# Optimization experiments

Hardware: AMD Instinct MI355X
Metric: run time of the kernel (lower is better)

Reference implementation:

```python
import jax, jax.numpy as jnp
import numpy as np

B, C, D, H, CS = 2, 1024, 512, 8, 64  # batch, bindings, d_binding, heads, chunk_size


def setup_inputs() -> dict:
    key = jax.random.key(0)
    ks = jax.random.split(key, 12)
    d = D // H
    def lin(k, out_f, in_f):
        return jax.random.normal(k, (out_f, in_f), jnp.float32) * (1.0 / np.sqrt(in_f))
    return {
        "x": jax.random.normal(ks[0], (B, C, D), jnp.float32),
        "Wq": lin(ks[1], D, D), "bq": jnp.zeros((D,), jnp.float32),
        "Wk": lin(ks[2], D, D), "bk": jnp.zeros((D,), jnp.float32),
        "Wv": lin(ks[3], D, D), "bv": jnp.zeros((D,), jnp.float32),
        "w1": lin(ks[4], d, 3 * d), "b1": jnp.zeros((d,), jnp.float32),
        "w2": lin(ks[5], 1, d), "b2": jnp.zeros((1,), jnp.float32),
        "Wo": lin(ks[6], D, D), "bo": jnp.zeros((D,), jnp.float32),
    }


def reference(x, Wq, bq, Wk, bk, Wv, bv, w1, b1, w2, b2, Wo, bo):
    Bx, Cx, Dx = x.shape
    d = Dx // H
    def heads(W, b):
        y = jnp.einsum('bcD,eD->bce', x, W) + b
        return y.reshape(Bx, Cx, H, d).transpose(0, 2, 1, 3)  # (B,H,C,d)
    q = heads(Wq, bq)
    k = heads(Wk, bk)
    v = heads(Wv, bv)
    # split first MLP layer weight into q / k / q*k blocks
    w1_q, w1_k, w1_qk = w1[:, :d], w1[:, d:2 * d], w1[:, 2 * d:]
    qp = jnp.einsum('bhcd,ed->bhce', q, w1_q)  # (B,H,C,d)
    kp = jnp.einsum('bhcd,ed->bhce', k, w1_k)  # (B,H,C,d)
    nc = Cx // CS
    q_ch = q.reshape(Bx, H, nc, CS, d).transpose(2, 0, 1, 3, 4)   # (nc,B,H,CS,d)
    qp_ch = qp.reshape(Bx, H, nc, CS, d).transpose(2, 0, 1, 3, 4)
    inv_sqrt_d = jnp.float32(1.0 / np.sqrt(d))

    def step(carry, xs):
        qc, qpc = xs  # (B,H,CS,d) each
        # hidden: (B,H,CS,C,d)
        res = qpc[:, :, :, None, :] + kp[:, :, None, :, :] + b1
        inter = qc[:, :, :, None, :] * k[:, :, None, :, :]
        hid = res + jnp.einsum('bhijd,ed->bhije', inter, w1_qk)
        h = jax.nn.gelu(hid, approximate=False)
        scores = (jnp.einsum('bhije,e->bhij', h, w2[0]) + b2[0]) * inv_sqrt_d
        attn = jax.nn.softmax(scores, axis=-1)  # (B,H,CS,C)
        out = jnp.einsum('bhij,bhjd->bhid', attn, v)  # (B,H,CS,d)
        return carry, out

    _, outs = jax.lax.scan(jax.checkpoint(step), None, (q_ch, qp_ch))  # (nc,B,H,CS,d)
    out = outs.transpose(1, 2, 0, 3, 4).reshape(Bx, H, Cx, d)
    out = out.transpose(0, 2, 1, 3).reshape(Bx, Cx, Dx)
    return jnp.einsum('bcD,eD->bce', out, Wo) + bo
```

## Files before the change

kernel.cpp:

```cpp
#include <hip/hip_runtime.h>
#include <cstdint>

typedef unsigned short u16;
typedef unsigned int u32;
typedef __attribute__((ext_vector_type(8))) short short8;
typedef __attribute__((ext_vector_type(4))) float floatx4;
typedef __attribute__((ext_vector_type(2))) float floatx2;

__device__ __forceinline__ float b2f(u16 u) {
    union { unsigned int i; float f; } c; c.i = ((unsigned int)u) << 16; return c.f;
}
__device__ __forceinline__ u16 f2b(float f) {
    union { float f; unsigned int i; } c; c.f = f;
    unsigned int u = c.i;
    u = u + 0x7FFFu + ((u >> 16) & 1u);
    return (u16)(u >> 16);
}
__device__ __forceinline__ float u2f(u32 u) { union { u32 u; float f; } c; c.u = u; return c.f; }

__device__ __forceinline__ void kstage(const u16* gsrc, u16* ldst) {
    __builtin_amdgcn_global_load_lds(
        (const __attribute__((address_space(1))) u32*)gsrc,
        (__attribute__((address_space(3))) u32*)ldst, 16, 0, 0);
}

__global__ __launch_bounds__(256) void gemm_qkv(
    const float* __restrict__ x,
    const float* __restrict__ Wq, const float* __restrict__ Wk, const float* __restrict__ Wv,
    const float* __restrict__ bq, const float* __restrict__ bk, const float* __restrict__ bv,
    float* __restrict__ qout, u16* __restrict__ kout,
    u16* __restrict__ vthi, u16* __restrict__ vtlo)
{
    __shared__ u16 xs[64 * 72];
    __shared__ u16 wsl[64 * 72];
    int tid = threadIdx.x;
    int lane = tid & 63;
    int wv = tid >> 6;
    int lo = lane & 15, hi = lane >> 4;
    int which = blockIdx.y >> 3;
    int m0 = blockIdx.x * 64, n0 = (blockIdx.y & 7) * 64;
    const float* W    = which == 0 ? Wq : (which == 1 ? Wk : Wv);
    const float* bias = which == 0 ? bq : (which == 1 ? bk : bv);

    floatx4 acc[4];
#pragma unroll
    for (int mt = 0; mt < 4; ++mt) acc[mt] = (floatx4){0.f, 0.f, 0.f, 0.f};

    for (int k0 = 0; k0 < 512; k0 += 64) {
        __syncthreads();
#pragma unroll
        for (int i = 0; i < 2; ++i) {
            int v = tid + i * 256;
            int row = v >> 3, c8 = (v & 7) * 8;
            const float* ap = x + (m0 + row) * 512 + k0 + c8;
            const float* wp = W + (n0 + row) * 512 + k0 + c8;
            float4 a0 = *(const float4*)(ap);
            float4 a1 = *(const float4*)(ap + 4);
            float4 w0 = *(const float4*)(wp);
            float4 w1v = *(const float4*)(wp + 4);
            union { u16 u[8]; uint4 q; } ca, cw;
            ca.u[0] = f2b(a0.x); ca.u[1] = f2b(a0.y); ca.u[2] = f2b(a0.z); ca.u[3] = f2b(a0.w);
            ca.u[4] = f2b(a1.x); ca.u[5] = f2b(a1.y); ca.u[6] = f2b(a1.z); ca.u[7] = f2b(a1.w);
            cw.u[0] = f2b(w0.x); cw.u[1] = f2b(w0.y); cw.u[2] = f2b(w0.z); cw.u[3] = f2b(w0.w);
            cw.u[4] = f2b(w1v.x); cw.u[5] = f2b(w1v.y); cw.u[6] = f2b(w1v.z); cw.u[7] = f2b(w1v.w);
            *(uint4*)(xs + row * 72 + c8)  = ca.q;
            *(uint4*)(wsl + row * 72 + c8) = cw.q;
        }
        __syncthreads();
#pragma unroll
        for (int ks = 0; ks < 2; ++ks) {
            short8 bfr = *(const short8*)(wsl + (wv * 16 + lo) * 72 + ks * 32 + hi * 8);
#pragma unroll
            for (int mt = 0; mt < 4; ++mt) {
                short8 afr = *(const short8*)(xs + (mt * 16 + lo) * 72 + ks * 32 + hi * 8);
                acc[mt] = __builtin_amdgcn_mfma_f32_16x16x32_bf16(afr, bfr, acc[mt], 0, 0, 0);
            }
        }
    }

    int n = n0 + wv * 16 + lo;
    float bv2 = bias[n];
    if (which == 2) {
        __syncthreads();
        int nl = wv * 16 + lo;
#pragma unroll
        for (int mt = 0; mt < 4; ++mt)
#pragma unroll
            for (int r = 0; r < 4; ++r) {
                int ml = mt * 16 + hi * 4 + r;
                float y = acc[mt][r] + bv2;
                u16 vh = f2b(y);
                u16 vl = f2b(y - b2f(vh));
                xs[nl * 72 + ml]  = vh;
                wsl[nl * 72 + ml] = vl;
            }
        __syncthreads();
        int row = tid >> 2, seg = (tid & 3) * 16;
        int b = m0 >> 10, c0 = m0 & 1023, h2 = n0 >> 6;
        size_t dst = ((size_t)((b * 8 + h2) * 64 + row)) * 1024 + c0 + seg;
        *(uint4*)(vthi + dst)     = *(uint4*)(xs  + row * 72 + seg);
        *(uint4*)(vthi + dst + 8) = *(uint4*)(xs  + row * 72 + seg + 8);
        *(uint4*)(vtlo + dst)     = *(uint4*)(wsl + row * 72 + seg);
        *(uint4*)(vtlo + dst + 8) = *(uint4*)(wsl + row * 72 + seg + 8);
    } else {
        int h = n >> 6, dd = n & 63;
#pragma unroll
        for (int mt = 0; mt < 4; ++mt)
#pragma unroll
            for (int r = 0; r < 4; ++r) {
                int m = m0 + mt * 16 + hi * 4 + r;
                float y = acc[mt][r] + bv2;
                int b = m >> 10, c = m & 1023;
                int idx = (((b * 8 + h) * 1024) + c) * 64 + dd;
                if (which == 0) qout[idx] = y;
                else            kout[idx] = f2b(y);
            }
    }
}

__global__ __launch_bounds__(256) void gemm_out(
    const float* __restrict__ A, const float* __restrict__ W, const float* __restrict__ bias,
    float* __restrict__ outf)
{
    __shared__ u16 xs[64 * 72];
    __shared__ u16 wsl[64 * 72];
    int tid = threadIdx.x;
    int lane = tid & 63;
    int wv = tid >> 6;
    int lo = lane & 15, hi = lane >> 4;
    int m0 = blockIdx.x * 64, n0 = blockIdx.y * 64;

    floatx4 acc[4];
#pragma unroll
    for (int mt = 0; mt < 4; ++mt) acc[mt] = (floatx4){0.f, 0.f, 0.f, 0.f};

    for (int k0 = 0; k0 < 512; k0 += 64) {
        __syncthreads();
#pragma unroll
        for (int i = 0; i < 2; ++i) {
            int v = tid + i * 256;
            int row = v >> 3, c8 = (v & 7) * 8;
            const float* ap = A + (m0 + row) * 512 + k0 + c8;
            const float* wp = W + (n0 + row) * 512 + k0 + c8;
            float4 a0 = *(const float4*)(ap);
            float4 a1 = *(const float4*)(ap + 4);
            float4 w0 = *(const float4*)(wp);
            float4 w1v = *(const float4*)(wp + 4);
            union { u16 u[8]; uint4 q; } ca, cw;
            ca.u[0] = f2b(a0.x); ca.u[1] = f2b(a0.y); ca.u[2] = f2b(a0.z); ca.u[3] = f2b(a0.w);
            ca.u[4] = f2b(a1.x); ca.u[5] = f2b(a1.y); ca.u[6] = f2b(a1.z); ca.u[7] = f2b(a1.w);
            cw.u[0] = f2b(w0.x); cw.u[1] = f2b(w0.y); cw.u[2] = f2b(w0.z); cw.u[3] = f2b(w0.w);
            cw.u[4] = f2b(w1v.x); cw.u[5] = f2b(w1v.y); cw.u[6] = f2b(w1v.z); cw.u[7] = f2b(w1v.w);
            *(uint4*)(xs + row * 72 + c8)  = ca.q;
            *(uint4*)(wsl + row * 72 + c8) = cw.q;
        }
        __syncthreads();
#pragma unroll
        for (int ks = 0; ks < 2; ++ks) {
            short8 bfr = *(const short8*)(wsl + (wv * 16 + lo) * 72 + ks * 32 + hi * 8);
#pragma unroll
            for (int mt = 0; mt < 4; ++mt) {
                short8 afr = *(const short8*)(xs + (mt * 16 + lo) * 72 + ks * 32 + hi * 8);
                acc[mt] = __builtin_amdgcn_mfma_f32_16x16x32_bf16(afr, bfr, acc[mt], 0, 0, 0);
            }
        }
    }

    int n = n0 + wv * 16 + lo;
    float bv = bias[n];
#pragma unroll
    for (int mt = 0; mt < 4; ++mt)
#pragma unroll
        for (int r = 0; r < 4; ++r) {
            int m = m0 + mt * 16 + hi * 4 + r;
            outf[m * 512 + n] = acc[mt][r] + bv;
        }
}

#define CHUNK_LOAD(BUFI)                                                       \
    {                                                                          \
        bf[0][0] = *(const short8*)(kr0 + (BUFI) * 2048);                      \
        bf[0][1] = *(const short8*)(kr1 + (BUFI) * 2048);                      \
        bf[1][0] = *(const short8*)(kr0 + (BUFI) * 2048 + 1024);               \
        bf[1][1] = *(const short8*)(kr1 + (BUFI) * 2048 + 1024);               \
        kstage(kg, kstg + (((BUFI) ^ 1) * 2048));                              \
        kg += 2048;                                                            \
    }

#define CHUNK_SCORE(CIDX)                                                      \
    {                                                                          \
        floatx2 s0v = (floatx2){0.f, 0.f};                                     \
        floatx2 s1v = (floatx2){0.f, 0.f};                                     \
        floatx4 aP[2], aN[2];                                                  \
        aP[0] = __builtin_amdgcn_mfma_f32_16x16x32_bf16(af[0][0], bf[0][0], qpinit[0], 0, 0, 0); \
        aP[0] = __builtin_amdgcn_mfma_f32_16x16x32_bf16(af[0][1], bf[0][1], aP[0], 0, 0, 0); \
        aP[1] = __builtin_amdgcn_mfma_f32_16x16x32_bf16(af[0][0], bf[1][0], qpinit[0], 0, 0, 0); \
        aP[1] = __builtin_amdgcn_mfma_f32_16x16x32_bf16(af[0][1], bf[1][1], aP[1], 0, 0, 0); \
        _Pragma("unroll")                                                      \
        for (int mt = 0; mt < 4; ++mt) {                                       \
            if (mt < 3) {                                                      \
                aN[0] = __builtin_amdgcn_mfma_f32_16x16x32_bf16(af[mt + 1][0], bf[0][0], qpinit[mt + 1], 0, 0, 0); \
                aN[0] = __builtin_amdgcn_mfma_f32_16x16x32_bf16(af[mt + 1][1], bf[0][1], aN[0], 0, 0, 0); \
                aN[1] = __builtin_amdgcn_mfma_f32_16x16x32_bf16(af[mt + 1][0], bf[1][0], qpinit[mt + 1], 0, 0, 0); \
                aN[1] = __builtin_amdgcn_mfma_f32_16x16x32_bf16(af[mt + 1][1], bf[1][1], aN[1], 0, 0, 0); \
            }                                                                  \
            _Pragma("unroll")                                                  \
            for (int h2 = 0; h2 < 2; ++h2) {                                   \
                u32 wp = wcp[mt][h2];                                          \
                floatx2 wv2 = (floatx2){u2f(wp << 16), u2f(wp & 0xFFFF0000u)}; \
                _Pragma("unroll")                                              \
                for (int t = 0; t < 2; ++t) {                                  \
                    floatx2 x = (floatx2){aP[t][h2 * 2 + 0], aP[t][h2 * 2 + 1]}; \
                    floatx2 ex = (floatx2){__builtin_amdgcn_exp2f(x.x),        \
                                           __builtin_amdgcn_exp2f(x.y)};       \
                    floatx2 a = ex + 1.0f;                                     \
                    float rc = __builtin_amdgcn_rcpf(a.x * a.y);               \
                    floatx2 sw = (floatx2){a.y, a.x};                          \
                    floatx2 contrib = (x * wv2) * (sw * rc);                   \
                    if (t == 0) s0v += contrib; else s1v += contrib;           \
                }                                                              \
            }                                                                  \
            aP[0] = aN[0];                                                     \
            aP[1] = aN[1];                                                     \
        }                                                                      \
        float s0 = s0v.x + s0v.y, s1 = s1v.x + s1v.y;                          \
        s0 += __shfl_xor(s0, 16); s0 += __shfl_xor(s0, 32);                    \
        s1 += __shfl_xor(s1, 16); s1 += __shfl_xor(s1, 32);                    \
        float p0 = __builtin_amdgcn_exp2f(s0 - 16.0f);                         \
        float p1 = __builtin_amdgcn_exp2f(s1 - 16.0f);                         \
        u16 ph0 = f2b(p0);                                                     \
        u16 ph1 = f2b(p1);                                                     \
        l_run += b2f(ph0) + b2f(ph1);                                          \
        u16* pw = gw + (CIDX) * 528;                                           \
        if (lane < 16) {                                                       \
            pw[((lo >> 3) * 16 + wv) * 8 + (lo & 7)] = ph0;                    \
            pw[((2 + (lo >> 3)) * 16 + wv) * 8 + (lo & 7)] = ph1;              \
        }                                                                      \
    }

#define PV_GROUP(PGW)                                                          \
    {                                                                          \
        const u16* vlp = vhp + (1u << 20);              \
        _Pragma("unroll")                                                      \
        for (int c2 = 0; c2 < 4; ++c2) {                                       \
            uint4 vh = *(const uint4*)(vhp + c2 * 32);                         \
            uint4 vl = *(const uint4*)(vlp + c2 * 32);                         \
            short8 pf = *(const short8*)((PGW) + c2 * 528 + lane * 8);         \
            pvacc = __builtin_amdgcn_mfma_f32_16x16x32_bf16(pf, *(short8*)&vh, pvacc, 0, 0, 0); \
            pvacc = __builtin_amdgcn_mfma_f32_16x16x32_bf16(pf, *(short8*)&vl, pvacc, 0, 0, 0); \
        }                                                                      \
        vhp += 128;                                                            \
    }

__global__ __launch_bounds__(256, 4) void attn24(
    const float* __restrict__ qf, const u16* __restrict__ kb,
    const u16* __restrict__ vthi, const u16* __restrict__ vtlo,
    const float* __restrict__ w1, const float* __restrict__ b1, const float* __restrict__ w2,
    float* __restrict__ ao)
{
    __shared__ float q_l[4 * 64];
    __shared__ __align__(16) u16 plds[2 * 4 * 528];
    __shared__ __align__(16) u16 kbuf[2 * 2048];
    __shared__ float l_sh[4];
    int tid = threadIdx.x;
    int lane = tid & 63;
    int wv = tid >> 6;
    int lo = lane & 15, hi = lane >> 4;
    int bh = blockIdx.x >> 8;
    int qbase = (blockIdx.x & 255) << 2;
    int qi = qbase | wv;

    const float NA = -2.45546696f;

    for (int i = tid; i < 2112; i += 256) ((u32*)plds)[i] = 0;

    q_l[wv * 64 + lane] = qf[(bh * 1024 + qi) * 64 + lane];

    float qpacc = b1[lane];
#pragma unroll
    for (int d8 = 0; d8 < 64; d8 += 8) {
        float4 wa = *(const float4*)(w1 + lane * 192 + d8);
        float4 wb = *(const float4*)(w1 + lane * 192 + d8 + 4);
        const float* q8 = q_l + wv * 64 + d8;
        qpacc = __builtin_fmaf(q8[0], wa.x, qpacc);
        qpacc = __builtin_fmaf(q8[1], wa.y, qpacc);
        qpacc = __builtin_fmaf(q8[2], wa.z, qpacc);
        qpacc = __builtin_fmaf(q8[3], wa.w, qpacc);
        qpacc = __builtin_fmaf(q8[4], wb.x, qpacc);
        qpacc = __builtin_fmaf(q8[5], wb.y, qpacc);
        qpacc = __builtin_fmaf(q8[6], wb.z, qpacc);
        qpacc = __builtin_fmaf(q8[7], wb.w, qpacc);
    }
    qpacc *= NA;

    u32 wcp[4][2];
    float w2row = w2[lane] * -0.07344288f;
#pragma unroll
    for (int mt = 0; mt < 4; ++mt)
#pragma unroll
        for (int h2 = 0; h2 < 2; ++h2) {
            int e0 = mt * 16 + hi * 4 + h2 * 2;
            u32 lo16 = (u32)f2b(__shfl(w2row, e0));
            u32 hi16 = (u32)f2b(__shfl(w2row, e0 + 1));
            wcp[mt][h2] = (hi16 << 16) | lo16;
        }

    float qv2[2][8];
#pragma unroll
    for (int ks = 0; ks < 2; ++ks)
#pragma unroll
        for (int j = 0; j < 8; ++j)
            qv2[ks][j] = q_l[wv * 64 + ks * 32 + hi * 8 + j];

    short8 af[4][2];
#pragma unroll
    for (int mt = 0; mt < 4; ++mt) {
        const float* wr = w1 + (mt * 16 + lo) * 192;
#pragma unroll
        for (int ks = 0; ks < 2; ++ks) {
            int dd0 = ks * 32 + hi * 8;
            float4 a0 = *(const float4*)(wr + 128 + dd0);
            float4 a1 = *(const float4*)(wr + 128 + dd0 + 4);
            float4 k0 = *(const float4*)(wr + 64 + dd0);
            float4 k1 = *(const float4*)(wr + 64 + dd0 + 4);
            union { u16 u[8]; short8 s; } cv;
            cv.u[0] = f2b(NA * __builtin_fmaf(qv2[ks][0], a0.x, k0.x));
            cv.u[1] = f2b(NA * __builtin_fmaf(qv2[ks][1], a0.y, k0.y));
            cv.u[2] = f2b(NA * __builtin_fmaf(qv2[ks][2], a0.z, k0.z));
            cv.u[3] = f2b(NA * __builtin_fmaf(qv2[ks][3], a0.w, k0.w));
            cv.u[4] = f2b(NA * __builtin_fmaf(qv2[ks][4], a1.x, k1.x));
            cv.u[5] = f2b(NA * __builtin_fmaf(qv2[ks][5], a1.y, k1.y));
            cv.u[6] = f2b(NA * __builtin_fmaf(qv2[ks][6], a1.z, k1.z));
            cv.u[7] = f2b(NA * __builtin_fmaf(qv2[ks][7], a1.w, k1.w));
            af[mt][ks] = cv.s;
        }
    }

    floatx4 qpinit[4];
    {
        const floatx4 z = (floatx4){0.f, 0.f, 0.f, 0.f};
        union { u16 u[8]; short8 s; } bb;
#pragma unroll
        for (int i = 0; i < 8; ++i) bb.u[i] = 0;
        bb.u[0] = (hi == 0) ? (u16)0x3F80 : (u16)0;
#pragma unroll
        for (int mt = 0; mt < 4; ++mt) {
            float qpv = __shfl(qpacc, mt * 16 + lo);
            union { u16 u[8]; short8 s; } aa;
#pragma unroll
            for (int i = 0; i < 8; ++i) aa.u[i] = 0;
            aa.u[0] = (hi == 0) ? f2b(qpv) : (u16)0;
            qpinit[mt] = __builtin_amdgcn_mfma_f32_16x16x32_bf16(aa.s, bb.s, z, 0, 0, 0);
        }
    }

    const u16* kg = kb + bh * 65536
                  + (wv * 8 + (lane >> 3)) * 64
                  + (((lane & 7) ^ (lane >> 3)) * 8);
    u16* kstg = kbuf + wv * 512;
    kstage(kg, kstg);
    kg += 2048;

    int ksw = hi ^ (lo & 7);
    const u16* kr0 = kbuf + lo * 64 + ksw * 8;
    const u16* kr1 = kbuf + lo * 64 + (ksw ^ 4) * 8;

    __syncthreads();

    float l_run = 0.f;
    floatx4 pvacc = (floatx4){0.f, 0.f, 0.f, 0.f};
    const u16* vhp = vthi + bh * 65536 + (wv * 16 + lo) * 1024 + hi * 8;
    short8 bf[2][2];

    for (int g = 0; g < 8; ++g) {
        u16* gw  = plds + (g & 1) * (4 * 528);
        u16* pgw = plds + ((g & 1) ^ 1) * (4 * 528);

        CHUNK_LOAD(0)
        if (g > 0) { PV_GROUP(pgw) }
        CHUNK_SCORE(0)
        __syncthreads();
        CHUNK_LOAD(1)
        CHUNK_SCORE(1)
        __syncthreads();
        CHUNK_LOAD(0)
        CHUNK_SCORE(2)
        __syncthreads();
        CHUNK_LOAD(1)
        CHUNK_SCORE(3)
        __syncthreads();
    }

    PV_GROUP(plds + (4 * 528))

    float l = l_run;
    l += __shfl_xor(l, 1); l += __shfl_xor(l, 2);
    l += __shfl_xor(l, 4); l += __shfl_xor(l, 8);
    if (lane == 0) l_sh[wv] = l;
    __syncthreads();

    if (hi == 0) {
        int b = bh >> 3, h = bh & 7;
#pragma unroll
        for (int q = 0; q < 4; ++q) {
            float outv = pvacc[q] * __builtin_amdgcn_rcpf(l_sh[q]);
            ao[((b * 1024 + qbase + q) * 512) + h * 64 + wv * 16 + lo] = outv;
        }
    }
}
#undef CHUNK_LOAD
#undef CHUNK_SCORE
#undef PV_GROUP

extern "C" void kernel_launch(void* const* d_in, const int* in_sizes, int n_in,
                              void* d_out, int out_size, void* d_ws, size_t ws_size,
                              hipStream_t stream)
{
    (void)in_sizes; (void)n_in; (void)out_size; (void)ws_size;
    const float* x  = (const float*)d_in[0];
    const float* Wq = (const float*)d_in[1];
    const float* bq = (const float*)d_in[2];
    const float* Wk = (const float*)d_in[3];
    const float* bk = (const float*)d_in[4];
    const float* Wv = (const float*)d_in[5];
    const float* bv = (const float*)d_in[6];
    const float* w1 = (const float*)d_in[7];
    const float* b1 = (const float*)d_in[8];
    const float* w2 = (const float*)d_in[9];
    const float* Wo = (const float*)d_in[11];
    const float* bo = (const float*)d_in[12];

    char* ws = (char*)d_ws;
    float* q_ws = (float*)(ws);
    u16*   k_ws = (u16*)(ws + (4u << 20));
    u16*   vthi = (u16*)(ws + (6u << 20));
    u16*   vtlo = (u16*)(ws + (8u << 20));
    float* a_ws = (float*)(ws + (10u << 20));

    dim3 blk(256);
    hipLaunchKernelGGL(gemm_qkv, dim3(32, 24), blk, 0, stream,
                       x, Wq, Wk, Wv, bq, bk, bv, q_ws, k_ws, vthi, vtlo);
    hipLaunchKernelGGL(attn24, dim3(4096), blk, 0, stream,
                       q_ws, k_ws, vthi, vtlo, w1, b1, w2, a_ws);
    hipLaunchKernelGGL(gemm_out, dim3(32, 8), blk, 0, stream, a_ws, Wo, bo, (float*)d_out);
}
```

Before: 449.1 us.

## Software-pipeline score tail (reduce, exp, P store) one chunk behind MFMA

```diff
diff --git a/kernel.cpp b/kernel.cpp
--- a/kernel.cpp
+++ b/kernel.cpp
@@ -187,7 +187,24 @@
         kg += 2048;                                                            \
     }
 
-#define CHUNK_SCORE(CIDX)                                                      \
+#define TAIL(BUF, PLANE)                                                       \
+    {                                                                          \
+        float t0 = s0p, t1 = s1p;                                              \
+        t0 += __shfl_xor(t0, 16); t0 += __shfl_xor(t0, 32);                    \
+        t1 += __shfl_xor(t1, 16); t1 += __shfl_xor(t1, 32);                    \
+        float p0 = __builtin_amdgcn_exp2f(t0 - 16.0f);                         \
+        float p1 = __builtin_amdgcn_exp2f(t1 - 16.0f);                         \
+        u16 ph0 = f2b(p0);                                                     \
+        u16 ph1 = f2b(p1);                                                     \
+        l_run += b2f(ph0) + b2f(ph1);                                          \
+        u16* pw = (BUF) + (PLANE) * 528;                                       \
+        if (lane < 16) {                                                       \
+            pw[((lo >> 3) * 16 + wv) * 8 + (lo & 7)] = ph0;                    \
+            pw[((2 + (lo >> 3)) * 16 + wv) * 8 + (lo & 7)] = ph1;              \
+        }                                                                      \
+    }
+
+#define CHUNK_SCORE                                                            \
     {                                                                          \
         floatx2 s0v = (floatx2){0.f, 0.f};                                     \
         floatx2 s1v = (floatx2){0.f, 0.f};                                     \
@@ -223,19 +240,8 @@
             aP[0] = aN[0];                                                     \
             aP[1] = aN[1];                                                     \
         }                                                                      \
-        float s0 = s0v.x + s0v.y, s1 = s1v.x + s1v.y;                          \
-        s0 += __shfl_xor(s0, 16); s0 += __shfl_xor(s0, 32);                    \
-        s1 += __shfl_xor(s1, 16); s1 += __shfl_xor(s1, 32);                    \
-        float p0 = __builtin_amdgcn_exp2f(s0 - 16.0f);                         \
-        float p1 = __builtin_amdgcn_exp2f(s1 - 16.0f);                         \
-        u16 ph0 = f2b(p0);                                                     \
-        u16 ph1 = f2b(p1);                                                     \
-        l_run += b2f(ph0) + b2f(ph1);                                          \
-        u16* pw = gw + (CIDX) * 528;                                           \
-        if (lane < 16) {                                                       \
-            pw[((lo >> 3) * 16 + wv) * 8 + (lo & 7)] = ph0;                    \
-            pw[((2 + (lo >> 3)) * 16 + wv) * 8 + (lo & 7)] = ph1;              \
-        }                                                                      \
+        s0p = s0v.x + s0v.y;                                                   \
+        s1p = s1v.x + s1v.y;                                                   \
     }
 
 #define PV_GROUP(PGW)                                                          \
@@ -252,7 +258,7 @@
         vhp += 128;                                                            \
     }
 
-__global__ __launch_bounds__(256, 4) void attn24(
+__global__ __launch_bounds__(256, 4) void attn25(
     const float* __restrict__ qf, const u16* __restrict__ kb,
     const u16* __restrict__ vthi, const u16* __restrict__ vtlo,
     const float* __restrict__ w1, const float* __restrict__ b1, const float* __restrict__ w2,
@@ -368,29 +374,36 @@
     __syncthreads();
 
     float l_run = 0.f;
+    float s0p = 0.f, s1p = 0.f;
     floatx4 pvacc = (floatx4){0.f, 0.f, 0.f, 0.f};
     const u16* vhp = vthi + bh * 65536 + (wv * 16 + lo) * 1024 + hi * 8;
     short8 bf[2][2];
 
     for (int g = 0; g < 8; ++g) {
-        u16* gw  = plds + (g & 1) * (4 * 528);
-        u16* pgw = plds + ((g & 1) ^ 1) * (4 * 528);
+        u16* gw = plds + (g & 1) * (4 * 528);
+        u16* ow = plds + ((g & 1) ^ 1) * (4 * 528);
 
         CHUNK_LOAD(0)
-        if (g > 0) { PV_GROUP(pgw) }
-        CHUNK_SCORE(0)
+        if (g > 0) { TAIL(ow, 3) }
+        CHUNK_SCORE
         __syncthreads();
         CHUNK_LOAD(1)
-        CHUNK_SCORE(1)
+        TAIL(gw, 0)
+        if (g > 0) { PV_GROUP(ow) }
+        CHUNK_SCORE
         __syncthreads();
         CHUNK_LOAD(0)
-        CHUNK_SCORE(2)
+        TAIL(gw, 1)
+        CHUNK_SCORE
         __syncthreads();
         CHUNK_LOAD(1)
-        CHUNK_SCORE(3)
-        __syncthreads();
-    }
-
+        TAIL(gw, 2)
+        CHUNK_SCORE
+        __syncthreads();
+    }
+
+    TAIL(plds + (4 * 528), 3)
+    __syncthreads();
     PV_GROUP(plds + (4 * 528))
 
     float l = l_run;
@@ -410,6 +423,7 @@
 }
 #undef CHUNK_LOAD
 #undef CHUNK_SCORE
+#undef TAIL
 #undef PV_GROUP
 
 extern "C" void kernel_launch(void* const* d_in, const int* in_sizes, int n_in,
@@ -440,7 +454,7 @@
     dim3 blk(256);
     hipLaunchKernelGGL(gemm_qkv, dim3(32, 24), blk, 0, stream,
                        x, Wq, Wk, Wv, bq, bk, bv, q_ws, k_ws, vthi, vtlo);
-    hipLaunchKernelGGL(attn24, dim3(4096), blk, 0, stream,
+    hipLaunchKernelGGL(attn25, dim3(4096), blk, 0, stream,
                        q_ws, k_ws, vthi, vtlo, w1, b1, w2, a_ws);
     hipLaunchKernelGGL(gemm_out, dim3(32, 8), blk, 0, stream, a_ws, Wo, bo, (float*)d_out);
 }
```

Result: slower. 470.1 us (+4.7%).
